# Optimization experiments

Hardware: AMD Instinct MI355X
Metric: run time of the kernel (lower is better)

The kernel has to match this reference:

```python
import jax, jax.numpy as jnp
import numpy as np
from jax import lax

IOU_THRESHOLD = 0.1
B, N = 4, 8192


def setup_inputs() -> dict:
    key = jax.random.key(0)
    # [B, 5, N]: rows 0..3 = cx, cy, w, h; row 4 = confidence score in (0, 1)
    outputs = jax.random.uniform(key, (B, 5, N), dtype=jnp.float32)
    return {"outputs": outputs}


def _nms_single(p):
    """Greedy NMS on one image. p: [5, N] -> [5, N] with kept boxes
    compacted to the front (original column order preserved) and the rest
    zero-padded. Matches the torch loop: repeatedly take the highest-scoring
    surviving box, drop all boxes with IoU >= threshold (box keeps itself),
    and drop boxes with score <= 0."""
    boxes, scores = p[:4], p[4]
    n = scores.shape[0]
    order = jnp.argsort(-scores)            # descending score order
    b = boxes[:, order]

    x1 = b[0] - b[2] * 0.5
    y1 = b[1] - b[3] * 0.5
    x2 = b[0] + b[2] * 0.5
    y2 = b[1] + b[3] * 0.5
    area = (x2 - x1) * (y2 - y1)

    iw = jnp.clip(jnp.minimum(x2[:, None], x2[None, :]) - jnp.maximum(x1[:, None], x1[None, :]), 0.0)
    ih = jnp.clip(jnp.minimum(y2[:, None], y2[None, :]) - jnp.maximum(y1[:, None], y1[None, :]), 0.0)
    inter = iw * ih
    union = area[:, None] + area[None, :] - inter
    iou = inter / (union + 1e-8)            # [N, N] in sorted order

    idx_range = jnp.arange(n)
    keep_init = scores[order] > 0           # non_zero_scores filter

    def body(i, keep):
        # if box i (in score order) survives, suppress j with IoU >= thr, j != i
        row_keep = (iou[i] < IOU_THRESHOLD) | (idx_range == i)
        return jnp.where(keep[i], keep & row_keep, keep)

    keep_sorted = lax.fori_loop(0, n, body, keep_init)

    # map keep mask back to original column order
    keep_orig = jnp.zeros((n,), bool).at[order].set(keep_sorted)
    # stable compaction: kept columns first, original relative order preserved
    perm = jnp.argsort(jnp.where(keep_orig, 0, 1), stable=True)
    gathered = p[:, perm]                    # [5, N]
    valid = idx_range < jnp.sum(keep_orig)
    return jnp.where(valid[None, :], gathered, 0.0)


def reference(outputs):
    # torch version pads to the max detections across the batch; here we keep
    # the fixed width N (extra columns are zero), same kept values/order.
    return jax.vmap(_nms_single)(outputs)


if __name__ == "__main__":
    inp = setup_inputs()
    out = jax.jit(reference)(**inp)
    print(out.shape, out.dtype)
```

## Files before the change

### kernel.cpp

```cpp
#include <hip/hip_runtime.h>

#pragma clang fp contract(off)

#define NBOX 8192
#define BLK  1024
#define EPT  8
#define NBUCK 2048
#define NB 256
#define IOU_THR 0.1f

typedef unsigned short u16;
typedef unsigned int u32;
typedef unsigned long long u64;

#define SMEM_TOT 160896

__global__ __launch_bounds__(BLK, 4) void nms_kernel(const float* __restrict__ in,
                                                     float* __restrict__ out) {
    __shared__ __align__(16) char smem[SMEM_TOT];
    const int img = blockIdx.x;
    const float* __restrict__ p = in + (size_t)img * 5 * NBOX;
    float* __restrict__ o = out + (size_t)img * 5 * NBOX;
    const int t = threadIdx.x;
    const int lane = t & 63;
    const int wid = t >> 6;

    float4* box   = (float4*)smem;
    u16* A        = (u16*)(smem + 131072);
    float4* bx    = (float4*)(smem + 147456);
    u64 (*mat)[4] = (u64(*)[4])(smem + 151552);
    float4* kx    = (float4*)(smem + 151552);
    u32* pfxA     = (u32*)(smem + 155648);
    u32* kom      = (u32*)(smem + 159744);
    int* wcnt     = (int*)(smem + 160768);
    u64* keptQ    = (u64*)(smem + 160832);
    int* S0sh     = (int*)(smem + 160864);
    u64* skey  = (u64*)smem;
    u32* hist  = (u32*)(smem + 65536);
    u32* bbase = (u32*)(smem + 73728);

    for (int i = t; i < NBUCK; i += BLK) hist[i] = 0;
    if (t < 256) kom[t] = 0;
    if (t == 0) *S0sh = 0;
    __syncthreads();

    u32 mybkt[EPT], myarr[EPT], mykeyhi[EPT];
#pragma unroll
    for (int e = 0; e < EPT; e++) {
        int j = t + e * BLK;
        float s = p[4 * NBOX + j];
        u32 u = __float_as_uint(s);
        u32 ordb = u ^ (u32)(((int)u >> 31) | (int)0x80000000);
        mykeyhi[e] = ~ordb;
        int vb = (int)(s * (float)NBUCK);
        vb = vb < 0 ? 0 : (vb > NBUCK - 1 ? NBUCK - 1 : vb);
        mybkt[e] = (u32)(NBUCK - 1 - vb);
        myarr[e] = atomicAdd(&hist[mybkt[e]], 1u);
        u64 bal = __ballot(s > 0.0f);
        if (lane == 0) atomicAdd(S0sh, (int)__popcll(bal));
    }
    __syncthreads();

    {
        u32 h0 = hist[2 * t], h1 = hist[2 * t + 1];
        int v = (int)(h0 + h1);
        int x = v;
        for (int d = 1; d < 64; d <<= 1) {
            int y = __shfl_up(x, d, 64);
            if (lane >= d) x += y;
        }
        if (lane == 63) wcnt[wid] = x;
        __syncthreads();
        int wb = 0;
        for (int i = 0; i < wid; i++) wb += wcnt[i];
        int excl = wb + x - v;
        bbase[2 * t] = (u32)excl;
        bbase[2 * t + 1] = (u32)excl + h0;
    }
    __syncthreads();

#pragma unroll
    for (int e = 0; e < EPT; e++) {
        u32 pos = bbase[mybkt[e]] + myarr[e];
        skey[pos] = ((u64)mykeyhi[e] << 32) | (u32)(t + e * BLK);
    }
    __syncthreads();

#pragma unroll
    for (int e = 0; e < EPT; e++) {
        u32 b = mybkt[e];
        u32 lo = bbase[b], hi2 = lo + hist[b];
        u64 me = ((u64)mykeyhi[e] << 32) | (u32)(t + e * BLK);
        u32 r = lo;
        for (u32 q = lo; q < hi2; q++) r += (skey[q] < me) ? 1u : 0u;
        A[r] = (u16)(t + e * BLK);
    }
    __syncthreads();
    int S = *S0sh;

#pragma unroll
    for (int e = 0; e < EPT; e++) {
        int j = t + e * BLK;
        float cx = p[j], cy = p[NBOX + j];
        float w_ = p[2 * NBOX + j], h_ = p[3 * NBOX + j];
        box[j] = make_float4(cx - w_ * 0.5f, cy - h_ * 0.5f,
                             cx + w_ * 0.5f, cy + h_ * 0.5f);
    }
    __syncthreads();

    if (t < NB) bx[t] = box[A[t]];
    __syncthreads();

    while (S > 0) {
        int nb = S < NB ? S : NB;

        {
            int i = t >> 2, ws = t & 3;
            if (i < nb) {
                float4 bi = bx[i];
                float ari = (bi.z - bi.x) * (bi.w - bi.y);
                u64 bits = 0;
                int c0 = ws * 64;
                int cmax = nb - c0; if (cmax > 64) cmax = 64;
                for (int cc = 0; cc < cmax; cc++) {
                    int c = c0 + cc;
                    float4 bc = bx[c];
                    float arc = (bc.z - bc.x) * (bc.w - bc.y);
                    float iw = fminf(bi.z, bc.z) - fmaxf(bi.x, bc.x);
                    float ih = fminf(bi.w, bc.w) - fmaxf(bi.y, bc.y);
                    if (c != i && iw > 0.0f && ih > 0.0f) {
                        float inter = iw * ih;
                        float uni = ari + arc - inter;
                        if (inter / (uni + 1e-8f) >= IOU_THR) bits |= (1ull << cc);
                    }
                }
                mat[i][ws] = bits;
            }
        }
        __syncthreads();

        if (wid == 0) {
            u64 r0[4], r1[4], r2[4], r3[4];
#pragma unroll
            for (int wq = 0; wq < 4; wq++) {
                r0[wq] = mat[lane][wq];
                r1[wq] = mat[64 + lane][wq];
                r2[wq] = mat[128 + lane][wq];
                r3[wq] = mat[192 + lane][wq];
            }
            u64 A0, A1, A2, A3;
            {
                int n0 = nb;       A0 = n0 <= 0 ? 0ull : (n0 >= 64 ? ~0ull : ((1ull << n0) - 1ull));
                int n1 = nb - 64;  A1 = n1 <= 0 ? 0ull : (n1 >= 64 ? ~0ull : ((1ull << n1) - 1ull));
                int n2 = nb - 128; A2 = n2 <= 0 ? 0ull : (n2 >= 64 ? ~0ull : ((1ull << n2) - 1ull));
                int n3 = nb - 192; A3 = n3 <= 0 ? 0ull : (n3 >= 64 ? ~0ull : ((1ull << n3) - 1ull));
            }
            u64 K0 = 0, K1 = 0, K2 = 0, K3 = 0;
            u64 lm = (1ull << lane) - 1ull;
            while (A0 | A1 | A2 | A3) {
                bool c0b = ((A0 >> lane) & 1) && !(r0[0] & A0 & lm);
                bool c1b = ((A1 >> lane) & 1) && !((r1[0] & A0) | (r1[1] & A1 & lm));
                bool c2b = ((A2 >> lane) & 1) && !((r2[0] & A0) | (r2[1] & A1) | (r2[2] & A2 & lm));
                bool c3b = ((A3 >> lane) & 1) && !((r3[0] & A0) | (r3[1] & A1) | (r3[2] & A2) | (r3[3] & A3 & lm));
                u64 C0 = __ballot(c0b), C1 = __ballot(c1b), C2 = __ballot(c2b), C3 = __ballot(c3b);
                K0 |= C0; K1 |= C1; K2 |= C2; K3 |= C3;
                A0 &= ~C0; A1 &= ~C1; A2 &= ~C2; A3 &= ~C3;
                bool s0b = ((A0 >> lane) & 1) && ((r0[0] & C0) | (r0[1] & C1) | (r0[2] & C2) | (r0[3] & C3));
                bool s1b = ((A1 >> lane) & 1) && ((r1[0] & C0) | (r1[1] & C1) | (r1[2] & C2) | (r1[3] & C3));
                bool s2b = ((A2 >> lane) & 1) && ((r2[0] & C0) | (r2[1] & C1) | (r2[2] & C2) | (r2[3] & C3));
                bool s3b = ((A3 >> lane) & 1) && ((r3[0] & C0) | (r3[1] & C1) | (r3[2] & C2) | (r3[3] & C3));
                A0 &= ~__ballot(s0b); A1 &= ~__ballot(s1b); A2 &= ~__ballot(s2b); A3 &= ~__ballot(s3b);
            }
            if (lane < 4) keptQ[lane] = lane == 0 ? K0 : lane == 1 ? K1 : lane == 2 ? K2 : K3;
        }
        __syncthreads();

        u64 kq0 = keptQ[0], kq1 = keptQ[1], kq2 = keptQ[2], kq3 = keptQ[3];
        int nk = (int)(__popcll(kq0) + __popcll(kq1) + __popcll(kq2) + __popcll(kq3));
        if (t < nb) {
            int wq = t >> 6;
            u64 kq = wq == 0 ? kq0 : wq == 1 ? kq1 : wq == 2 ? kq2 : kq3;
            if ((kq >> (t & 63)) & 1) {
                int j = (int)A[t];
                atomicOr(&kom[j >> 5], 1u << (j & 31));
                int pk = 0;
                if (wq > 0) pk += (int)__popcll(kq0);
                if (wq > 1) pk += (int)__popcll(kq1);
                if (wq > 2) pk += (int)__popcll(kq2);
                pk += (int)__popcll(kq & ((1ull << (t & 63)) - 1ull));
                kx[pk] = bx[t];
            }
        }
        int tailN = S - nb;
        int C = (tailN + BLK - 1) / BLK;
        int st = nb + t * C;
        int en = st + C; if (en > S) en = S;
        float4 eb[EPT]; float ea[EPT]; u16 ei[EPT];
        u32 am = 0;
#pragma unroll
        for (int e = 0; e < EPT; e++) {
            int pos = st + e;
            if (e < C && pos < en) {
                u16 j = A[pos];
                ei[e] = j;
                float4 b = box[j];
                eb[e] = b;
                ea[e] = (b.z - b.x) * (b.w - b.y);
                am |= (1u << e);
            }
        }
        __syncthreads();

        if (am) {
            for (int c = 0; c < nk; c++) {
                float4 cb = kx[c];
                float arc = (cb.z - cb.x) * (cb.w - cb.y);
#pragma unroll
                for (int e = 0; e < EPT; e++) {
                    if (am & (1u << e)) {
                        float iw = fminf(eb[e].z, cb.z) - fmaxf(eb[e].x, cb.x);
                        float ih = fminf(eb[e].w, cb.w) - fmaxf(eb[e].y, cb.y);
                        if (iw > 0.0f && ih > 0.0f) {
                            float inter = iw * ih;
                            float uni = ea[e] + arc - inter;
                            if (inter / (uni + 1e-8f) >= IOU_THR) am &= ~(1u << e);
                        }
                    }
                }
                if (!am) break;
            }
        }

        {
            int cnt = __popc(am);
            int x = cnt;
            for (int d = 1; d < 64; d <<= 1) {
                int y = __shfl_up(x, d, 64);
                if (lane >= d) x += y;
            }
            if (lane == 63) wcnt[wid] = x;
            __syncthreads();
            int wb = 0, tot = 0;
            for (int i = 0; i < BLK / 64; i++) {
                int v = wcnt[i];
                if (i < wid) wb += v;
                tot += v;
            }
            int off = wb + x - cnt;
#pragma unroll
            for (int e = 0; e < EPT; e++) {
                if (am & (1u << e)) {
                    A[off] = ei[e];
                    if (off < NB) bx[off] = eb[e];
                    off++;
                }
            }
            __syncthreads();
            S = tot;
        }
    }
    __syncthreads();

    {
        float4 z; z.x = z.y = z.z = z.w = 0.0f;
        float4* o4 = (float4*)o;
        for (int i = t; i < 5 * NBOX / 4; i += BLK) o4[i] = z;
    }
    {
        u32 w = (t < 256) ? kom[t] : 0u;
        int c = __popc(w);
        int x = c;
        for (int d = 1; d < 64; d <<= 1) {
            int y = __shfl_up(x, d, 64);
            if (lane >= d) x += y;
        }
        if (lane == 63) wcnt[wid] = x;
        __syncthreads();
        int wb = 0;
        for (int i = 0; i < wid; i++) wb += wcnt[i];
        if (t < 256) pfxA[t] = (u32)(wb + x - c);
    }
    __syncthreads();
    for (int j = t; j < NBOX; j += BLK) {
        u32 km = kom[j >> 5];
        if ((km >> (j & 31)) & 1u) {
            int pos = (int)(pfxA[j >> 5] + (u32)__popc(km & ((1u << (j & 31)) - 1u)));
            o[0 * NBOX + pos] = p[0 * NBOX + j];
            o[1 * NBOX + pos] = p[1 * NBOX + j];
            o[2 * NBOX + pos] = p[2 * NBOX + j];
            o[3 * NBOX + pos] = p[3 * NBOX + j];
            o[4 * NBOX + pos] = p[4 * NBOX + j];
        }
    }
}

extern "C" void kernel_launch(void* const* d_in, const int* in_sizes, int n_in,
                              void* d_out, int out_size, void* d_ws, size_t ws_size,
                              hipStream_t stream) {
    const float* in = (const float*)d_in[0];
    float* out = (float*)d_out;
    int B = in_sizes[0] / (5 * NBOX);
    hipLaunchKernelGGL(nms_kernel, dim3(B), dim3(BLK), 0, stream, in, out);
}
```

Baseline: 185.1 us.

## Compute only lower-triangle IoU for head block, replace division with double compare

The per-iteration IoU matrix for the head block now computes only pairs c < i (the lower triangle), splitting each row's range evenly across four threads and merging bits with shared-memory atomicOr. This roughly halves the pairwise work and balances load. The float division is replaced by a multiply-compare in double against the float threshold constant, meant to reproduce the division result. Kept boxes are recorded as indices into bx instead of copied float4s, and zeroing of the output is moved to kernel start so it overlaps the sort. The trade-offs are extra atomics, double-precision math, a mat clear every iteration, and a possible mismatch against the reference at rounding boundaries.

```diff
diff --git a/kernel.cpp b/kernel.cpp
--- a/kernel.cpp
+++ b/kernel.cpp
@@ -13,7 +13,9 @@
 typedef unsigned int u32;
 typedef unsigned long long u64;
 
-#define SMEM_TOT 160896
+#define MND 0x1.999999p-4
+
+#define SMEM_TOT 161408
 
 __global__ __launch_bounds__(BLK, 4) void nms_kernel(const float* __restrict__ in,
                                                      float* __restrict__ out) {
@@ -29,15 +31,22 @@
     u16* A        = (u16*)(smem + 131072);
     float4* bx    = (float4*)(smem + 147456);
     u64 (*mat)[4] = (u64(*)[4])(smem + 151552);
-    float4* kx    = (float4*)(smem + 151552);
-    u32* pfxA     = (u32*)(smem + 155648);
+    u32* pfxA     = (u32*)(smem + 151552);
     u32* kom      = (u32*)(smem + 159744);
     int* wcnt     = (int*)(smem + 160768);
     u64* keptQ    = (u64*)(smem + 160832);
     int* S0sh     = (int*)(smem + 160864);
+    u16* kidx     = (u16*)(smem + 160872);
     u64* skey  = (u64*)smem;
     u32* hist  = (u32*)(smem + 65536);
     u32* bbase = (u32*)(smem + 73728);
+
+    {
+        float4 z; z.x = z.y = z.z = z.w = 0.0f;
+        float4* o4 = (float4*)o;
+#pragma unroll
+        for (int e = 0; e < 10; e++) o4[t + e * BLK] = z;
+    }
 
     for (int i = t; i < NBUCK; i += BLK) hist[i] = 0;
     if (t < 256) kom[t] = 0;
@@ -109,32 +118,38 @@
     __syncthreads();
 
     if (t < NB) bx[t] = box[A[t]];
+    ((u64*)mat)[t] = 0;
     __syncthreads();
 
     while (S > 0) {
         int nb = S < NB ? S : NB;
 
         {
-            int i = t >> 2, ws = t & 3;
-            if (i < nb) {
-                float4 bi = bx[i];
-                float ari = (bi.z - bi.x) * (bi.w - bi.y);
-                u64 bits = 0;
-                int c0 = ws * 64;
-                int cmax = nb - c0; if (cmax > 64) cmax = 64;
-                for (int cc = 0; cc < cmax; cc++) {
-                    int c = c0 + cc;
-                    float4 bc = bx[c];
-                    float arc = (bc.z - bc.x) * (bc.w - bc.y);
-                    float iw = fminf(bi.z, bc.z) - fmaxf(bi.x, bc.x);
-                    float ih = fminf(bi.w, bc.w) - fmaxf(bi.y, bc.y);
-                    if (c != i && iw > 0.0f && ih > 0.0f) {
+            int i = t >> 2, q = t & 3;
+            if (i > 0 && i < nb) {
+                int clo = (i * q) >> 2;
+                int chi = (i * (q + 1)) >> 2;
+                if (chi > clo) {
+                    float4 bi = bx[i];
+                    float ari = (bi.z - bi.x) * (bi.w - bi.y);
+                    u64 acc = 0;
+                    for (int c = clo; c < chi; c++) {
+                        float4 bc = bx[c];
+                        float arc = (bc.z - bc.x) * (bc.w - bc.y);
+                        float iw = fmaxf(fminf(bi.z, bc.z) - fmaxf(bi.x, bc.x), 0.0f);
+                        float ih = fmaxf(fminf(bi.w, bc.w) - fmaxf(bi.y, bc.y), 0.0f);
                         float inter = iw * ih;
-                        float uni = ari + arc - inter;
-                        if (inter / (uni + 1e-8f) >= IOU_THR) bits |= (1ull << cc);
+                        float t2 = (ari + arc) - inter;
+                        float uu = t2 + 1e-8f;
+                        if ((double)inter > MND * (double)uu) acc |= (1ull << (c - clo));
+                    }
+                    if (acc) {
+                        int w0 = clo >> 6, sh = clo & 63;
+                        atomicOr(&mat[i][w0], acc << sh);
+                        if (sh && (((chi - 1) >> 6) != w0))
+                            atomicOr(&mat[i][w0 + 1], acc >> (64 - sh));
                     }
                 }
-                mat[i][ws] = bits;
             }
         }
         __syncthreads();
@@ -175,6 +190,7 @@
         }
         __syncthreads();
 
+        ((u64*)mat)[t] = 0;
         u64 kq0 = keptQ[0], kq1 = keptQ[1], kq2 = keptQ[2], kq3 = keptQ[3];
         int nk = (int)(__popcll(kq0) + __popcll(kq1) + __popcll(kq2) + __popcll(kq3));
         if (t < nb) {
@@ -188,7 +204,7 @@
                 if (wq > 1) pk += (int)__popcll(kq1);
                 if (wq > 2) pk += (int)__popcll(kq2);
                 pk += (int)__popcll(kq & ((1ull << (t & 63)) - 1ull));
-                kx[pk] = bx[t];
+                kidx[pk] = (u16)t;
             }
         }
         int tailN = S - nb;
@@ -213,7 +229,7 @@
 
         if (am) {
             for (int c = 0; c < nk; c++) {
-                float4 cb = kx[c];
+                float4 cb = bx[kidx[c]];
                 float arc = (cb.z - cb.x) * (cb.w - cb.y);
 #pragma unroll
                 for (int e = 0; e < EPT; e++) {
@@ -222,8 +238,9 @@
                         float ih = fminf(eb[e].w, cb.w) - fmaxf(eb[e].y, cb.y);
                         if (iw > 0.0f && ih > 0.0f) {
                             float inter = iw * ih;
-                            float uni = ea[e] + arc - inter;
-                            if (inter / (uni + 1e-8f) >= IOU_THR) am &= ~(1u << e);
+                            float t2 = (ea[e] + arc) - inter;
+                            float uu = t2 + 1e-8f;
+                            if ((double)inter > MND * (double)uu) am &= ~(1u << e);
                         }
                     }
                 }
@@ -261,11 +278,6 @@
     }
     __syncthreads();
 
-    {
-        float4 z; z.x = z.y = z.z = z.w = 0.0f;
-        float4* o4 = (float4*)o;
-        for (int i = t; i < 5 * NBOX / 4; i += BLK) o4[i] = z;
-    }
     {
         u32 w = (t < 256) ? kom[t] : 0u;
         int c = __popc(w);
```

New measurement: 158.8 us. 1.17x faster.
